# Kernel tuning notes

Measured on AMD Instinct MI355X. Metric: run time of the kernel, lower is better.

The kernel has to match this reference:

```python
import jax, jax.numpy as jnp
import numpy as np

B, D, C = 8192, 1024, 4096  # batch, d_model, num_clusters (all active)
EPS = 1e-12  # matches F.normalize eps


def _l2_normalize(x):
    n = jnp.linalg.norm(x, axis=-1, keepdims=True)
    return x / jnp.maximum(n, EPS)


def setup_inputs() -> dict:
    key = jax.random.key(0)
    k1, k2 = jax.random.split(key)
    embedding = jax.random.normal(k1, (B, D), dtype=jnp.float32)
    centroids = jax.random.normal(k2, (C, D), dtype=jnp.float32)  # buffer, all active
    return {"embedding": embedding, "centroids": centroids}


def reference(embedding, centroids):
    # Fused equivalent of the per-centroid Python loop:
    # cosine sim of normalized embedding vs each normalized centroid.
    emb_n = _l2_normalize(embedding)        # [B, D]
    cen_n = _l2_normalize(centroids)        # [C, D]
    sims = jnp.clip(emb_n @ cen_n.T, 0.0, 1.0)  # [B, C], per-sim clamp to [0,1]
    max_sim = jnp.max(sims, axis=-1)        # [B]
    closest = jnp.argmax(sims, axis=-1)     # [B] int
    novelty = jnp.clip(jnp.sqrt(1.0 - max_sim), 0.0, 1.0)  # [B]
    return novelty, closest
```

## Files before the change

### kernel.cpp

```cpp
#include <hip/hip_runtime.h>
#include <math.h>

#define B_ROWS 8192
#define C_COLS 4096
#define D_DIM  1024
#define EPSN   1e-12f

typedef float v4f __attribute__((ext_vector_type(4)));
typedef short v8s __attribute__((ext_vector_type(8)));

__device__ __forceinline__ unsigned short bf16_rtn(float x) {
    unsigned int u = __float_as_uint(x);
    u += 0x7fffu + ((u >> 16) & 1u);
    return (unsigned short)(u >> 16);
}

__device__ __forceinline__ bool better_vi(float v, int i, float V, int I) {
    return (v > V) || (v == V && i < I);
}

__global__ __launch_bounds__(256) void prep_kernel(
    const float* __restrict__ emb, const float* __restrict__ cen,
    unsigned short* __restrict__ Ah, unsigned short* __restrict__ Bh,
    float* __restrict__ inv_a, float* __restrict__ inv_b)
{
    const int lane = threadIdx.x & 63;
    const int wid  = blockIdx.x * 4 + (threadIdx.x >> 6);
    const float* src; unsigned short* dst; float* invp; int r;
    if (wid < B_ROWS) { src = emb; r = wid;          dst = Ah; invp = inv_a; }
    else              { src = cen; r = wid - B_ROWS; dst = Bh; invp = inv_b; }

    const float* rp = src + (size_t)r * D_DIM;
    float4 v[4];
    float ss = 0.0f;
    #pragma unroll
    for (int j = 0; j < 4; ++j) {
        v[j] = *(const float4*)(rp + (j * 64 + lane) * 4);
        ss += v[j].x * v[j].x + v[j].y * v[j].y + v[j].z * v[j].z + v[j].w * v[j].w;
    }
    #pragma unroll
    for (int off = 1; off < 64; off <<= 1) ss += __shfl_xor(ss, off, 64);

    const float iv = 1.0f / fmaxf(sqrtf(ss), EPSN);
    if (lane == 0) invp[r] = iv;

    unsigned short* dp = dst + (size_t)r * D_DIM;
    #pragma unroll
    for (int j = 0; j < 4; ++j) {
        ushort4 H;
        H.x = bf16_rtn(v[j].x * iv);
        H.y = bf16_rtn(v[j].y * iv);
        H.z = bf16_rtn(v[j].z * iv);
        H.w = bf16_rtn(v[j].w * iv);
        *(ushort4*)(dp + (j * 64 + lane) * 4) = H;
    }
}

#define GLD16(gp, lp) \
    __builtin_amdgcn_global_load_lds( \
        (const __attribute__((address_space(1))) void*)(gp), \
        (__attribute__((address_space(3))) void*)(lp), 16, 0, 0)

__global__ __launch_bounds__(512, 2) void simmax_kernel(
    const unsigned short* __restrict__ Ahg, const unsigned short* __restrict__ Bhg,
    float* __restrict__ p1v, int* __restrict__ p1i,
    float* __restrict__ p2v, int* __restrict__ p2i)
{
    __shared__ unsigned short lds[3 * 24576];

    const int tid    = threadIdx.x;
    const int L      = tid & 63;
    const int w      = tid >> 6;
    const int lane15 = L & 15;
    const int quad   = L >> 4;
    const int wr     = w >> 2;
    const int wc     = w & 3;
    const int row0   = blockIdx.x * 128;
    const int c0     = blockIdx.y * 256;

    const int scol = (tid & 7) ^ ((tid >> 3) & 7);
    const unsigned short* aB = Ahg + (size_t)(row0 + (tid >> 3)) * D_DIM + scol * 8;
    const unsigned short* bB = Bhg + (size_t)(c0   + (tid >> 3)) * D_DIM + scol * 8;
    const int wofs = w * 512;

#define STAGE3A(bo, kb) do { \
    GLD16(aB + (kb),           &lds[(bo) + wofs]);           \
    GLD16(aB + 65536 + (kb),   &lds[(bo) + 4096  + wofs]);   \
    GLD16(bB + (kb),           &lds[(bo) + 8192  + wofs]);   \
} while (0)
#define STAGE3B(bo, kb) do { \
    GLD16(bB + 65536 + (kb),   &lds[(bo) + 12288 + wofs]);   \
    GLD16(bB + 131072 + (kb),  &lds[(bo) + 16384 + wofs]);   \
    GLD16(bB + 196608 + (kb),  &lds[(bo) + 20480 + wofs]);   \
} while (0)

    v4f acc[4][4];
    #pragma unroll
    for (int mt = 0; mt < 4; ++mt)
        #pragma unroll
        for (int nt = 0; nt < 4; ++nt) acc[mt][nt] = (v4f)0.0f;

    int rAo[4], rBo[4];
    #pragma unroll
    for (int t = 0; t < 4; ++t) {
        rAo[t] = (wr * 64 + t * 16 + lane15) * 64;
        rBo[t] = 8192 + (wc * 64 + t * 16 + lane15) * 64;
    }
    const int s7  = lane15 & 7;
    const int cq0 = (quad ^ s7) * 8;
    const int cq1 = ((4 + quad) ^ s7) * 8;

    STAGE3A(0, 0);      STAGE3B(0, 0);
    STAGE3A(24576, 64); STAGE3B(24576, 64);
    asm volatile("s_waitcnt vmcnt(6)" ::: "memory");
    __builtin_amdgcn_s_barrier();

    int bo_c = 0, bo_n = 24576, bo_n2 = 49152;
    for (int t = 0; t < 16; ++t) {
        const bool pf  = (t + 2 < 16);
        const int  kb2 = (t + 2) * 64;

        v8s fb[4][2], fa[2][2];
        #pragma unroll
        for (int nt = 0; nt < 4; ++nt) {
            fb[nt][0] = *(const v8s*)&lds[bo_c + rBo[nt] + cq0];
            fb[nt][1] = *(const v8s*)&lds[bo_c + rBo[nt] + cq1];
        }
        #pragma unroll
        for (int mt = 0; mt < 2; ++mt) {
            fa[mt][0] = *(const v8s*)&lds[bo_c + rAo[mt] + cq0];
            fa[mt][1] = *(const v8s*)&lds[bo_c + rAo[mt] + cq1];
        }
        if (pf) STAGE3A(bo_n2, kb2);
        __builtin_amdgcn_s_barrier();
        asm volatile("s_waitcnt lgkmcnt(0)" ::: "memory");
        __builtin_amdgcn_sched_barrier(0);
        __builtin_amdgcn_s_setprio(1);
        #pragma unroll
        for (int kk = 0; kk < 2; ++kk)
            #pragma unroll
            for (int mt = 0; mt < 2; ++mt)
                #pragma unroll
                for (int nt = 0; nt < 4; ++nt)
                    acc[mt][nt] = __builtin_amdgcn_mfma_f32_16x16x32_bf16(
                        fa[mt][kk], fb[nt][kk], acc[mt][nt], 0, 0, 0);
        __builtin_amdgcn_s_setprio(0);
        __builtin_amdgcn_s_barrier();

        v8s fa2[2][2];
        #pragma unroll
        for (int mt = 0; mt < 2; ++mt) {
            fa2[mt][0] = *(const v8s*)&lds[bo_c + rAo[2 + mt] + cq0];
            fa2[mt][1] = *(const v8s*)&lds[bo_c + rAo[2 + mt] + cq1];
        }
        if (pf) STAGE3B(bo_n2, kb2);
        __builtin_amdgcn_s_barrier();
        asm volatile("s_waitcnt lgkmcnt(0)" ::: "memory");
        __builtin_amdgcn_sched_barrier(0);
        __builtin_amdgcn_s_setprio(1);
        #pragma unroll
        for (int kk = 0; kk < 2; ++kk)
            #pragma unroll
            for (int mt = 0; mt < 2; ++mt)
                #pragma unroll
                for (int nt = 0; nt < 4; ++nt)
                    acc[2 + mt][nt] = __builtin_amdgcn_mfma_f32_16x16x32_bf16(
                        fa2[mt][kk], fb[nt][kk], acc[2 + mt][nt], 0, 0, 0);
        __builtin_amdgcn_s_setprio(0);

        if (t < 15) {
            if (pf) asm volatile("s_waitcnt vmcnt(6)" ::: "memory");
            else    asm volatile("s_waitcnt vmcnt(0)" ::: "memory");
            __builtin_amdgcn_s_barrier();
        }
        const int tb = bo_c; bo_c = bo_n; bo_n = bo_n2; bo_n2 = tb;
    }

    const int pc = blockIdx.y * 4 + wc;
    #pragma unroll
    for (int mt = 0; mt < 4; ++mt) {
        #pragma unroll
        for (int r = 0; r < 4; ++r) {
            float a1v = acc[mt][0][r];
            int   a1i = c0 + wc * 64 + 0 * 16 + lane15;
            float a2v = -1e30f;
            int   a2i = 0x7fffffff;
            #pragma unroll
            for (int nt = 1; nt < 4; ++nt) {
                float v  = acc[mt][nt][r];
                int   ci = c0 + wc * 64 + nt * 16 + lane15;
                if (better_vi(v, ci, a1v, a1i))      { a2v = a1v; a2i = a1i; a1v = v; a1i = ci; }
                else if (better_vi(v, ci, a2v, a2i)) { a2v = v;   a2i = ci; }
            }
            #pragma unroll
            for (int off = 8; off; off >>= 1) {
                float b1v = __shfl_down(a1v, off, 64); int b1i = __shfl_down(a1i, off, 64);
                float b2v = __shfl_down(a2v, off, 64); int b2i = __shfl_down(a2i, off, 64);
                if (better_vi(b1v, b1i, a1v, a1i)) {
                    if (better_vi(a1v, a1i, b2v, b2i)) { a2v = a1v; a2i = a1i; }
                    else                               { a2v = b2v; a2i = b2i; }
                    a1v = b1v; a1i = b1i;
                } else if (better_vi(b1v, b1i, a2v, a2i)) {
                    a2v = b1v; a2i = b1i;
                }
            }
            if (lane15 == 0) {
                int rg = row0 + wr * 64 + mt * 16 + quad * 4 + r;
                size_t ix = (size_t)rg * 64 + pc;
                p1v[ix] = a1v; p1i[ix] = a1i;
                p2v[ix] = a2v; p2i[ix] = a2i;
            }
        }
    }
}

__global__ __launch_bounds__(256) void finalize_kernel(
    const float* __restrict__ emb, const float* __restrict__ cen,
    const float* __restrict__ inv_a, const float* __restrict__ inv_b,
    const float* __restrict__ p1v, const int* __restrict__ p1i,
    const float* __restrict__ p2v, const int* __restrict__ p2i,
    float* __restrict__ out)
{
    const int lane = threadIdx.x & 63;
    const int row  = blockIdx.x * 4 + (threadIdx.x >> 6);
    const size_t base = (size_t)row * 64 + lane;

    float v[4]; int ix[4];
    v[0] = p1v[base]; ix[0] = p1i[base];
    v[1] = p2v[base]; ix[1] = p2i[base];
    v[2] = -1e30f;    ix[2] = 0x7ffffffe;
    v[3] = -1e30f;    ix[3] = 0x7fffffff;

    #pragma unroll
    for (int off = 1; off < 64; off <<= 1) {
        float ov[4]; int oi[4];
        #pragma unroll
        for (int k = 0; k < 4; ++k) {
            ov[k] = __shfl_xor(v[k],  off, 64);
            oi[k] = __shfl_xor(ix[k], off, 64);
        }
        #pragma unroll
        for (int k = 0; k < 4; ++k) {
            float bv = ov[k]; int bi = oi[k];
            bool b0 = better_vi(bv, bi, v[0], ix[0]);
            bool b1 = better_vi(bv, bi, v[1], ix[1]);
            bool b2 = better_vi(bv, bi, v[2], ix[2]);
            bool b3 = better_vi(bv, bi, v[3], ix[3]);
            float nv3 = b2 ? v[2] : (b3 ? bv : v[3]); int ni3 = b2 ? ix[2] : (b3 ? bi : ix[3]);
            float nv2 = b1 ? v[1] : (b2 ? bv : v[2]); int ni2 = b1 ? ix[1] : (b2 ? bi : ix[2]);
            float nv1 = b0 ? v[0] : (b1 ? bv : v[1]); int ni1 = b0 ? ix[0] : (b1 ? bi : ix[1]);
            float nv0 = b0 ? bv   : v[0];             int ni0 = b0 ? bi    : ix[0];
            v[0] = nv0; ix[0] = ni0; v[1] = nv1; ix[1] = ni1;
            v[2] = nv2; ix[2] = ni2; v[3] = nv3; ix[3] = ni3;
        }
    }

    const float* er = emb + (size_t)row * D_DIM;
    const float* cr0 = cen + (size_t)ix[0] * D_DIM;
    const float* cr1 = cen + (size_t)ix[1] * D_DIM;
    const float* cr2 = cen + (size_t)ix[2] * D_DIM;
    const float* cr3 = cen + (size_t)ix[3] * D_DIM;

    float d[4] = { 0.0f, 0.0f, 0.0f, 0.0f };
    #pragma unroll
    for (int j = 0; j < 4; ++j) {
        int e = (j * 64 + lane) * 4;
        float4 ev = *(const float4*)(er  + e);
        float4 c0 = *(const float4*)(cr0 + e);
        float4 c1 = *(const float4*)(cr1 + e);
        float4 c2 = *(const float4*)(cr2 + e);
        float4 c3 = *(const float4*)(cr3 + e);
        d[0] += ev.x * c0.x + ev.y * c0.y + ev.z * c0.z + ev.w * c0.w;
        d[1] += ev.x * c1.x + ev.y * c1.y + ev.z * c1.z + ev.w * c1.w;
        d[2] += ev.x * c2.x + ev.y * c2.y + ev.z * c2.z + ev.w * c2.w;
        d[3] += ev.x * c3.x + ev.y * c3.y + ev.z * c3.z + ev.w * c3.w;
    }
    #pragma unroll
    for (int off = 1; off < 64; off <<= 1) {
        #pragma unroll
        for (int c = 0; c < 4; ++c) d[c] += __shfl_xor(d[c], off, 64);
    }

    if (lane == 0) {
        const float ia = inv_a[row];
        float m = -1e30f; int ci = 0x7fffffff;
        #pragma unroll
        for (int c = 0; c < 4; ++c) {
            float s = d[c] * ia * inv_b[ix[c]];
            if (better_vi(s, ix[c], m, ci)) { m = s; ci = ix[c]; }
        }
        if (m <= 0.0f) ci = 0;
        float ms = fminf(fmaxf(m, 0.0f), 1.0f);
        out[row]          = fminf(fmaxf(sqrtf(1.0f - ms), 0.0f), 1.0f);
        out[B_ROWS + row] = (float)ci;
    }
}

extern "C" void kernel_launch(void* const* d_in, const int* in_sizes, int n_in,
                              void* d_out, int out_size, void* d_ws, size_t ws_size,
                              hipStream_t stream)
{
    const float* emb = (const float*)d_in[0];
    const float* cen = (const float*)d_in[1];
    float* out = (float*)d_out;

    unsigned short* Ahp = (unsigned short*)d_ws;
    unsigned short* Bhp = Ahp + (size_t)B_ROWS * D_DIM;
    float* inv_a = (float*)(Bhp + (size_t)C_COLS * D_DIM);
    float* inv_b = inv_a + B_ROWS;
    float* p1v   = inv_b + C_COLS;
    int*   p1i   = (int*)(p1v + (size_t)64 * B_ROWS);
    float* p2v   = (float*)(p1i + (size_t)64 * B_ROWS);
    int*   p2i   = (int*)(p2v + (size_t)64 * B_ROWS);

    prep_kernel<<<(B_ROWS + C_COLS) / 4, 256, 0, stream>>>(emb, cen, Ahp, Bhp, inv_a, inv_b);

    dim3 grid(B_ROWS / 128, C_COLS / 256);
    simmax_kernel<<<grid, 512, 0, stream>>>(Ahp, Bhp, p1v, p1i, p2v, p2i);

    finalize_kernel<<<B_ROWS / 4, 256, 0, stream>>>(emb, cen, inv_a, inv_b,
                                                    p1v, p1i, p2v, p2i, out);
}
```

Measured before the change: 232.1 us.

## Enlarge GEMM tile to 256x256 with double-buffered four-phase pipeline

The similarity GEMM tile grows from 128x256 to 256x256 rows per block, so each wave holds 8x4 accumulator tiles and reuses B fragments across twice as many rows. This cuts global and LDS traffic per flop. The pipeline changes from triple buffering of a 128x256 tile to double buffering of a 256x256 tile. Each K step is split into four phases that interleave the prefetches with the MFMA groups. The cost is more accumulator registers (likely one block per CU instead of two under the launch bounds) and a shallower prefetch depth, which may expose load latency.

```diff
diff --git a/kernel.cpp b/kernel.cpp
--- a/kernel.cpp
+++ b/kernel.cpp
@@ -66,7 +66,7 @@
     float* __restrict__ p1v, int* __restrict__ p1i,
     float* __restrict__ p2v, int* __restrict__ p2i)
 {
-    __shared__ unsigned short lds[3 * 24576];
+    __shared__ unsigned short lds[2 * 32768];
 
     const int tid    = threadIdx.x;
     const int L      = tid & 63;
@@ -75,7 +75,7 @@
     const int quad   = L >> 4;
     const int wr     = w >> 2;
     const int wc     = w & 3;
-    const int row0   = blockIdx.x * 128;
+    const int row0   = blockIdx.x * 256;
     const int c0     = blockIdx.y * 256;
 
     const int scol = (tid & 7) ^ ((tid >> 3) & 7);
@@ -83,102 +83,117 @@
     const unsigned short* bB = Bhg + (size_t)(c0   + (tid >> 3)) * D_DIM + scol * 8;
     const int wofs = w * 512;
 
-#define STAGE3A(bo, kb) do { \
-    GLD16(aB + (kb),           &lds[(bo) + wofs]);           \
-    GLD16(aB + 65536 + (kb),   &lds[(bo) + 4096  + wofs]);   \
-    GLD16(bB + (kb),           &lds[(bo) + 8192  + wofs]);   \
-} while (0)
-#define STAGE3B(bo, kb) do { \
-    GLD16(bB + 65536 + (kb),   &lds[(bo) + 12288 + wofs]);   \
-    GLD16(bB + 131072 + (kb),  &lds[(bo) + 16384 + wofs]);   \
-    GLD16(bB + 196608 + (kb),  &lds[(bo) + 20480 + wofs]);   \
-} while (0)
-
-    v4f acc[4][4];
-    #pragma unroll
-    for (int mt = 0; mt < 4; ++mt)
+#define STG(ptr, off, dst) GLD16((ptr) + (off), &lds[(dst) + wofs])
+#define STAGE_P0(bo, kb) do { STG(bB, (kb),            (bo) + 16384); \
+                              STG(bB, 65536  + (kb),   (bo) + 20480); } while (0)
+#define STAGE_P1(bo, kb) do { STG(bB, 131072 + (kb),   (bo) + 24576); \
+                              STG(bB, 196608 + (kb),   (bo) + 28672); } while (0)
+#define STAGE_P2(bo, kb) do { STG(aB, (kb),            (bo) + 0);     \
+                              STG(aB, 131072 + (kb),   (bo) + 8192);  } while (0)
+#define STAGE_P3(bo, kb) do { STG(aB, 65536  + (kb),   (bo) + 4096);  \
+                              STG(aB, 196608 + (kb),   (bo) + 12288); } while (0)
+
+    v4f acc[8][4];
+    #pragma unroll
+    for (int mt = 0; mt < 8; ++mt)
         #pragma unroll
         for (int nt = 0; nt < 4; ++nt) acc[mt][nt] = (v4f)0.0f;
 
-    int rAo[4], rBo[4];
+    int rA[4], rB[4];
     #pragma unroll
     for (int t = 0; t < 4; ++t) {
-        rAo[t] = (wr * 64 + t * 16 + lane15) * 64;
-        rBo[t] = 8192 + (wc * 64 + t * 16 + lane15) * 64;
+        rA[t] = (wr * 128 + t * 16 + lane15) * 64;
+        rB[t] = 16384 + (wc * 64 + t * 16 + lane15) * 64;
     }
     const int s7  = lane15 & 7;
     const int cq0 = (quad ^ s7) * 8;
     const int cq1 = ((4 + quad) ^ s7) * 8;
 
-    STAGE3A(0, 0);      STAGE3B(0, 0);
-    STAGE3A(24576, 64); STAGE3B(24576, 64);
-    asm volatile("s_waitcnt vmcnt(6)" ::: "memory");
+    STAGE_P0(0, 0); STAGE_P1(0, 0); STAGE_P2(0, 0); STAGE_P3(0, 0);
+    asm volatile("s_waitcnt vmcnt(2)" ::: "memory");
     __builtin_amdgcn_s_barrier();
 
-    int bo_c = 0, bo_n = 24576, bo_n2 = 49152;
+    int bo_c = 0, bo_n = 32768;
     for (int t = 0; t < 16; ++t) {
-        const bool pf  = (t + 2 < 16);
-        const int  kb2 = (t + 2) * 64;
-
-        v8s fb[4][2], fa[2][2];
-        #pragma unroll
-        for (int nt = 0; nt < 4; ++nt) {
-            fb[nt][0] = *(const v8s*)&lds[bo_c + rBo[nt] + cq0];
-            fb[nt][1] = *(const v8s*)&lds[bo_c + rBo[nt] + cq1];
-        }
-        #pragma unroll
-        for (int mt = 0; mt < 2; ++mt) {
-            fa[mt][0] = *(const v8s*)&lds[bo_c + rAo[mt] + cq0];
-            fa[mt][1] = *(const v8s*)&lds[bo_c + rAo[mt] + cq1];
-        }
-        if (pf) STAGE3A(bo_n2, kb2);
+        const bool pf  = (t < 15);
+        const int  kb1 = (t + 1) * 64;
+
+        v8s fb0[4], fb1[4], fx[4];
+
+        #pragma unroll
+        for (int nt = 0; nt < 4; ++nt) fb0[nt] = *(const v8s*)&lds[bo_c + rB[nt] + cq0];
+        #pragma unroll
+        for (int m = 0; m < 4; ++m)    fx[m]   = *(const v8s*)&lds[bo_c + rA[m] + cq0];
+        if (pf) STAGE_P0(bo_n, kb1);
         __builtin_amdgcn_s_barrier();
         asm volatile("s_waitcnt lgkmcnt(0)" ::: "memory");
         __builtin_amdgcn_sched_barrier(0);
         __builtin_amdgcn_s_setprio(1);
         #pragma unroll
-        for (int kk = 0; kk < 2; ++kk)
-            #pragma unroll
-            for (int mt = 0; mt < 2; ++mt)
-                #pragma unroll
-                for (int nt = 0; nt < 4; ++nt)
-                    acc[mt][nt] = __builtin_amdgcn_mfma_f32_16x16x32_bf16(
-                        fa[mt][kk], fb[nt][kk], acc[mt][nt], 0, 0, 0);
+        for (int m = 0; m < 4; ++m)
+            #pragma unroll
+            for (int nt = 0; nt < 4; ++nt)
+                acc[m][nt] = __builtin_amdgcn_mfma_f32_16x16x32_bf16(fx[m], fb0[nt], acc[m][nt], 0, 0, 0);
         __builtin_amdgcn_s_setprio(0);
         __builtin_amdgcn_s_barrier();
 
-        v8s fa2[2][2];
-        #pragma unroll
-        for (int mt = 0; mt < 2; ++mt) {
-            fa2[mt][0] = *(const v8s*)&lds[bo_c + rAo[2 + mt] + cq0];
-            fa2[mt][1] = *(const v8s*)&lds[bo_c + rAo[2 + mt] + cq1];
-        }
-        if (pf) STAGE3B(bo_n2, kb2);
+        #pragma unroll
+        for (int nt = 0; nt < 4; ++nt) fb1[nt] = *(const v8s*)&lds[bo_c + rB[nt] + cq1];
+        #pragma unroll
+        for (int m = 0; m < 4; ++m)    fx[m]   = *(const v8s*)&lds[bo_c + rA[m] + cq1];
+        if (pf) STAGE_P1(bo_n, kb1);
         __builtin_amdgcn_s_barrier();
         asm volatile("s_waitcnt lgkmcnt(0)" ::: "memory");
         __builtin_amdgcn_sched_barrier(0);
         __builtin_amdgcn_s_setprio(1);
         #pragma unroll
-        for (int kk = 0; kk < 2; ++kk)
-            #pragma unroll
-            for (int mt = 0; mt < 2; ++mt)
-                #pragma unroll
-                for (int nt = 0; nt < 4; ++nt)
-                    acc[2 + mt][nt] = __builtin_amdgcn_mfma_f32_16x16x32_bf16(
-                        fa2[mt][kk], fb[nt][kk], acc[2 + mt][nt], 0, 0, 0);
+        for (int m = 0; m < 4; ++m)
+            #pragma unroll
+            for (int nt = 0; nt < 4; ++nt)
+                acc[m][nt] = __builtin_amdgcn_mfma_f32_16x16x32_bf16(fx[m], fb1[nt], acc[m][nt], 0, 0, 0);
         __builtin_amdgcn_s_setprio(0);
-
-        if (t < 15) {
-            if (pf) asm volatile("s_waitcnt vmcnt(6)" ::: "memory");
-            else    asm volatile("s_waitcnt vmcnt(0)" ::: "memory");
+        if (pf) asm volatile("s_waitcnt vmcnt(4)" ::: "memory");
+        else    asm volatile("s_waitcnt vmcnt(0)" ::: "memory");
+        __builtin_amdgcn_s_barrier();
+
+        #pragma unroll
+        for (int m = 0; m < 4; ++m)    fx[m] = *(const v8s*)&lds[bo_c + rA[m] + 4096 + cq0];
+        if (pf) STAGE_P2(bo_n, kb1);
+        __builtin_amdgcn_s_barrier();
+        asm volatile("s_waitcnt lgkmcnt(0)" ::: "memory");
+        __builtin_amdgcn_sched_barrier(0);
+        __builtin_amdgcn_s_setprio(1);
+        #pragma unroll
+        for (int m = 0; m < 4; ++m)
+            #pragma unroll
+            for (int nt = 0; nt < 4; ++nt)
+                acc[4 + m][nt] = __builtin_amdgcn_mfma_f32_16x16x32_bf16(fx[m], fb0[nt], acc[4 + m][nt], 0, 0, 0);
+        __builtin_amdgcn_s_setprio(0);
+        __builtin_amdgcn_s_barrier();
+
+        #pragma unroll
+        for (int m = 0; m < 4; ++m)    fx[m] = *(const v8s*)&lds[bo_c + rA[m] + 4096 + cq1];
+        if (pf) STAGE_P3(bo_n, kb1);
+        __builtin_amdgcn_s_barrier();
+        asm volatile("s_waitcnt lgkmcnt(0)" ::: "memory");
+        __builtin_amdgcn_sched_barrier(0);
+        __builtin_amdgcn_s_setprio(1);
+        #pragma unroll
+        for (int m = 0; m < 4; ++m)
+            #pragma unroll
+            for (int nt = 0; nt < 4; ++nt)
+                acc[4 + m][nt] = __builtin_amdgcn_mfma_f32_16x16x32_bf16(fx[m], fb1[nt], acc[4 + m][nt], 0, 0, 0);
+        __builtin_amdgcn_s_setprio(0);
+        if (pf) {
+            asm volatile("s_waitcnt vmcnt(2)" ::: "memory");
             __builtin_amdgcn_s_barrier();
         }
-        const int tb = bo_c; bo_c = bo_n; bo_n = bo_n2; bo_n2 = tb;
+        const int tb = bo_c; bo_c = bo_n; bo_n = tb;
     }
 
     const int pc = blockIdx.y * 4 + wc;
     #pragma unroll
-    for (int mt = 0; mt < 4; ++mt) {
+    for (int mt = 0; mt < 8; ++mt) {
         #pragma unroll
         for (int r = 0; r < 4; ++r) {
             float a1v = acc[mt][0][r];
@@ -205,7 +220,7 @@
                 }
             }
             if (lane15 == 0) {
-                int rg = row0 + wr * 64 + mt * 16 + quad * 4 + r;
+                int rg = row0 + wr * 128 + mt * 16 + quad * 4 + r;
                 size_t ix = (size_t)rg * 64 + pc;
                 p1v[ix] = a1v; p1i[ix] = a1i;
                 p2v[ix] = a2v; p2i[ix] = a2i;
@@ -315,7 +330,7 @@
 
     prep_kernel<<<(B_ROWS + C_COLS) / 4, 256, 0, stream>>>(emb, cen, Ahp, Bhp, inv_a, inv_b);
 
-    dim3 grid(B_ROWS / 128, C_COLS / 256);
+    dim3 grid(B_ROWS / 256, C_COLS / 256);
     simmax_kernel<<<grid, 512, 0, stream>>>(Ahp, Bhp, p1v, p1i, p2v, p2i);
 
     finalize_kernel<<<B_ROWS / 4, 256, 0, stream>>>(emb, cen, inv_a, inv_b,
```

After: 222.2 us. 1.04x faster.
